# Performance work log

Measured on AMD Instinct MI355X. Metric: run time of the kernel, lower is better.

Reference implementation:

```python
import jax, jax.numpy as jnp
import numpy as np

DIM = 64
HEADS = 4            # self.num_heads = 2 * num_heads(=2)
SMK = 5
KS = 7
EPS = 1e-5
SCALE = (DIM // HEADS) ** -0.5


def pool_mat(n, out=7):
    # AdaptiveAvgPool2d bin matrix: P[i, j] = 1/size if floor(i*n/out) <= j < ceil((i+1)*n/out)
    P = np.zeros((out, n), np.float32)
    for i in range(out):
        s = (i * n) // out
        e = -((-(i + 1) * n) // out)
        P[i, s:e] = 1.0 / (e - s)
    return jnp.asarray(P)


def bn(x, g, b, m, v):
    # inference BatchNorm2d on [B,C,H,W]
    return (x - m[:, None, None]) * (g[:, None, None] * jax.lax.rsqrt(v[:, None, None] + EPS)) + b[:, None, None]


def conv1x1(x, w):
    return jnp.einsum('oi,bihw->bohw', w, x)


def rpb_bias(rpb, H, W, k):
    # replicate apply_rpb gather indexing (incl. the flip over flattened HW)
    rs = 2 * k - 1
    ih0 = np.arange(k)
    idx_k = (ih0[:, None] * rs + ih0[None, :]).reshape(-1)        # [k*k]
    rh = np.ones(k, np.int64); rh[k // 2] = H - (k - 1)
    rw = np.ones(k, np.int64); rw[k // 2] = W - (k - 1)
    ih = np.repeat(ih0, rh)                                       # [H]
    iw = np.repeat(ih0, rw)                                       # [W]
    bias_hw = ih[:, None] * rs + iw[None, :]                      # [H,W]
    bias_idx = (bias_hw[..., None] + idx_k).reshape(-1, k * k)[::-1].copy()  # [H*W,k*k]
    flat = rpb.reshape(rpb.shape[0], -1)                          # [G, rs*rs]
    return flat[:, bias_idx].reshape(1, rpb.shape[0], H, W, k * k)


def na2d_av(attn, value, k):
    # NATTEN-style neighborhood AV: window start clamped to stay in-bounds
    B, G, H, W, _ = attn.shape
    si = np.clip(np.arange(H) - k // 2, 0, H - k)
    sj = np.clip(np.arange(W) - k // 2, 0, W - k)
    ii = si[:, None] + np.arange(k)    # [H,k]
    jj = sj[:, None] + np.arange(k)    # [W,k]
    v = value[:, :, ii][:, :, :, :, jj]         # [B,G,H,k,W,k,C]
    a = attn.reshape(B, G, H, W, k, k)
    return jnp.einsum('bghwij,bghiwjc->bghwc', a, v)


def reference(x, wq_w, wq_g, wq_b, wq_m, wq_v,
              wk_w, wk_g, wk_b, wk_m, wk_v,
              proj_w, proj_b, rpb1, rpb2,
              dy_w, dy_g, dy_b, dy_m, dy_v):
    B, C, H, W = x.shape
    G = HEADS
    q, kctx = jnp.split(x, 2, axis=1)                      # [B,C/2,H,W] each
    q = bn(conv1x1(q, wq_w), wq_g, wq_b, wq_m, wq_v) * SCALE
    Ph, Pw = pool_mat(H), pool_mat(W)
    kp = jnp.einsum('ph,bchw,qw->bcpq', Ph, kctx, Pw)      # adaptive avg pool to 7x7
    k = bn(conv1x1(kp, wk_w), wk_g, wk_b, wk_m, wk_v)
    q = q.reshape(B, G, -1, H * W)                          # b g c n
    k = k.reshape(B, G, -1, 49)                             # b g c l
    w = jnp.einsum('bgcn,bgcl->bgnl', q, k)
    w = w.transpose(0, 3, 1, 2)                             # b l g n
    w = jnp.einsum('ol,blgn->bogn', proj_w, w) + proj_b[None, :, None, None]  # b (74) g n
    w = w.transpose(0, 2, 3, 1).reshape(B, G, H, W, SMK * SMK + KS * KS)
    attn1 = w[..., :SMK * SMK]
    attn2 = w[..., SMK * SMK:]
    attn1 = jax.nn.softmax(attn1 + rpb_bias(rpb1, H, W, SMK), axis=-1)
    attn2 = jax.nn.softmax(attn2 + rpb_bias(rpb2, H, W, KS), axis=-1)
    c = C // (2 * G)
    value = x.reshape(B, 2, G, c, H, W).transpose(1, 0, 2, 4, 5, 3)  # m b g h w c
    x1 = na2d_av(attn1, value[0], SMK)
    x2 = na2d_av(attn2, value[1], KS)
    out = jnp.concatenate([x1, x2], axis=1)                 # b (2g) h w c
    out = out.transpose(0, 1, 4, 2, 3).reshape(B, C, H, W)  # b (g c) h w
    return bn(conv1x1(out, dy_w), dy_g, dy_b, dy_m, dy_v)


def setup_inputs() -> dict:
    key = jax.random.key(0)
    ks = jax.random.split(key, 20)
    h = DIM // 2
    def bnp(k):
        k1, k2, k3, k4 = jax.random.split(k, 4)
        return (jax.random.uniform(k1, (0,)),)  # unused
    inp = {
        'x': jax.random.normal(ks[0], (8, DIM, 64, 64), jnp.float32),
        'wq_w': jax.random.normal(ks[1], (h, h), jnp.float32) * (h ** -0.5),
        'wq_g': jax.random.uniform(ks[2], (h,), jnp.float32, 0.5, 1.5),
        'wq_b': jax.random.normal(ks[3], (h,), jnp.float32) * 0.1,
        'wq_m': jax.random.normal(ks[4], (h,), jnp.float32) * 0.1,
        'wq_v': jax.random.uniform(ks[5], (h,), jnp.float32, 0.5, 1.5),
        'wk_w': jax.random.normal(ks[6], (h, h), jnp.float32) * (h ** -0.5),
        'wk_g': jax.random.uniform(ks[7], (h,), jnp.float32, 0.5, 1.5),
        'wk_b': jax.random.normal(ks[8], (h,), jnp.float32) * 0.1,
        'wk_m': jax.random.normal(ks[9], (h,), jnp.float32) * 0.1,
        'wk_v': jax.random.uniform(ks[10], (h,), jnp.float32, 0.5, 1.5),
        'proj_w': jax.random.normal(ks[11], (SMK * SMK + KS * KS, 49), jnp.float32) * (49 ** -0.5),
        'proj_b': jax.random.normal(ks[12], (SMK * SMK + KS * KS,), jnp.float32) * 0.02,
        'rpb1': jax.random.normal(ks[13], (HEADS, 2 * SMK - 1, 2 * SMK - 1), jnp.float32) * 0.02,
        'rpb2': jax.random.normal(ks[14], (HEADS, 2 * KS - 1, 2 * KS - 1), jnp.float32) * 0.02,
        'dy_w': jax.random.normal(ks[15], (DIM, DIM), jnp.float32) * (DIM ** -0.5),
        'dy_g': jax.random.uniform(ks[16], (DIM,), jnp.float32, 0.5, 1.5),
        'dy_b': jax.random.normal(ks[17], (DIM,), jnp.float32) * 0.1,
        'dy_m': jax.random.normal(ks[18], (DIM,), jnp.float32) * 0.1,
        'dy_v': jax.random.uniform(ks[19], (DIM,), jnp.float32, 0.5, 1.5),
    }
    return inp
```

## Files before the change

kernel.cpp:

```cpp
#include <hip/hip_runtime.h>

#define EPSV 1e-5f

#define OFF_W    12544
#define OFF_WQ2  31488
#define OFF_Q0   32512
#define OFF_DYT  32544

typedef float f4u __attribute__((ext_vector_type(4), aligned(4)));

__global__ __launch_bounds__(256) void pool_prep_kernel(
    const float* __restrict__ x,
    const float* __restrict__ wk_w, const float* __restrict__ wk_g,
    const float* __restrict__ wk_b, const float* __restrict__ wk_m,
    const float* __restrict__ wk_v,
    const float* __restrict__ wq_w, const float* __restrict__ wq_g,
    const float* __restrict__ wq_b, const float* __restrict__ wq_m,
    const float* __restrict__ wq_v,
    const float* __restrict__ dy_w,
    float* __restrict__ ws)
{
  __shared__ float s_tmp[32 * 64];
  __shared__ float s_kp[32 * 7];
  const int tid = threadIdx.x;

  if (blockIdx.x >= 56) {
    const int t = (blockIdx.x - 56) * 256 + tid;
    for (int idx = t; idx < 1056; idx += 2048) {
      if (idx < 1024) {
        const int i = idx >> 5, o = idx & 31;
        const float s = wq_g[o] * rsqrtf(wq_v[o] + EPSV);
        ws[OFF_WQ2 + idx] = 0.25f * s * wq_w[o * 32 + i];
      } else {
        const int o = idx - 1024;
        const float s = wq_g[o] * rsqrtf(wq_v[o] + EPSV);
        ws[OFF_Q0 + o] = 0.25f * (wq_b[o] - wq_m[o] * s);
      }
    }
    for (int idx = t; idx < 4096; idx += 2048) {
      const int i = idx >> 6, o = idx & 63;
      ws[OFF_DYT + idx] = dy_w[o * 64 + i];
    }
    return;
  }

  const int b = blockIdx.x / 7;
  const int p = blockIdx.x % 7;
  const int sh = (p * 64) / 7, eh = ((p + 1) * 64 + 6) / 7;
  const float invH = 1.0f / (float)(eh - sh);
  for (int idx = tid; idx < 2048; idx += 256) {
    const int c = idx >> 6, ww = idx & 63;
    const float* xp = x + ((size_t)(b * 64 + 32 + c)) * 4096 + ww;
    float s = 0.f;
    for (int hh = sh; hh < eh; ++hh) s += xp[hh * 64];
    s_tmp[idx] = s * invH;
  }
  __syncthreads();
  if (tid < 224) {
    const int c = tid / 7, q = tid % 7;
    const int sw = (q * 64) / 7, ew = ((q + 1) * 64 + 6) / 7;
    float s = 0.f;
    for (int ww = sw; ww < ew; ++ww) s += s_tmp[c * 64 + ww];
    s_kp[c * 7 + q] = s / (float)(ew - sw);
  }
  __syncthreads();
  if (tid < 224) {
    const int o = tid / 7, q = tid % 7;
    float s = 0.f;
#pragma unroll
    for (int i = 0; i < 32; i++) s += wk_w[o * 32 + i] * s_kp[i * 7 + q];
    const float sc = wk_g[o] * rsqrtf(wk_v[o] + EPSV);
    const int g = o >> 3, c = o & 7, l = p * 7 + q;
    ws[(((size_t)b * 4 + g) * 8 + c) * 49 + l] = (s - wk_m[o]) * sc + wk_b[o];
  }
}

__global__ __launch_bounds__(256) void fold_w_kernel(
    const float* __restrict__ proj_w, const float* __restrict__ ws_in,
    float* __restrict__ Wout)
{
  const int bg = blockIdx.x;
  const int tid = threadIdx.x;
  __shared__ float s_k[392];
  for (int i = tid; i < 392; i += 256) s_k[i] = ws_in[(size_t)bg * 392 + i];
  __syncthreads();
  for (int idx = tid; idx < 592; idx += 256) {
    const int o = idx >> 3, c = idx & 7;
    float s = 0.f;
#pragma unroll
    for (int l = 0; l < 49; l++) s += proj_w[o * 49 + l] * s_k[c * 49 + l];
    Wout[(size_t)bg * 592 + idx] = s;
  }
}

__global__ __launch_bounds__(512, 3) void contmix_main(
    const float* __restrict__ x,
    const float* __restrict__ proj_b,
    const float* __restrict__ rpb1, const float* __restrict__ rpb2,
    const float* __restrict__ dy_g, const float* __restrict__ dy_b,
    const float* __restrict__ dy_m, const float* __restrict__ dy_v,
    const float* __restrict__ ws,
    float* __restrict__ out)
{
  __shared__ float s_rpb1[4 * 81];
  __shared__ float s_rpb2[4 * 169];
  __shared__ float s_val[64 * 64];

  const int bx = blockIdx.x;
  const int b = bx >> 6;
  const int h = bx & 63;
  const int tid = threadIdx.x;
  const int w = tid & 63;
  const int bru = __builtin_amdgcn_readfirstlane(tid >> 8);
  const int gu  = __builtin_amdgcn_readfirstlane((tid >> 6) & 3);

  for (int i = tid; i < 324; i += 512) s_rpb1[i] = rpb1[i];
  for (int i = tid; i < 676; i += 512) s_rpb2[i] = rpb2[i];
  __syncthreads();

  const float* xb = x + (size_t)b * 64 * 4096;

  float q8[8];
  {
    const float* q0 = ws + OFF_Q0 + gu * 8;
#pragma unroll
    for (int o = 0; o < 8; o++) q8[o] = q0[o];
    const float* wq2 = ws + OFF_WQ2 + gu * 8;
#pragma unroll
    for (int i = 0; i < 32; i++) {
      const float xv = xb[i * 4096 + h * 64 + w];
#pragma unroll
      for (int o = 0; o < 8; o++) q8[o] += wq2[i * 32 + o] * xv;
    }
  }

  const float* Wr = ws + OFF_W + (size_t)(b * 4 + gu) * 592;
  const int ph = 63 - h, pw = 63 - w;

  if (bru == 0) {
    const int bih5 = ph - min(max(ph - 2, 0), 59);
    const int biw5 = pw - min(max(pw - 2, 0), 59);
    const int si5 = min(max(h - 2, 0), 59), sj5 = min(max(w - 2, 0), 59);
    float l1[25];
#pragma unroll
    for (int o = 0; o < 25; o++) {
      const float* wo = Wr + o * 8;
      float s = proj_b[o];
#pragma unroll
      for (int c = 0; c < 8; c++) s += wo[c] * q8[c];
      l1[o] = s;
    }
    const float* rp1 = s_rpb1 + gu * 81 + bih5 * 9 + biw5;
#pragma unroll
    for (int ki = 0; ki < 5; ki++)
#pragma unroll
      for (int kj = 0; kj < 5; kj++) l1[ki * 5 + kj] += rp1[ki * 9 + kj];

    float p0 = 0.f, p1 = 0.f, p2 = 0.f, p3 = 0.f;
#pragma unroll
    for (int o = 0; o < 25; o++) {
      const float e = __expf(l1[o]);
      l1[o] = e;
      if ((o & 3) == 0) p0 += e;
      else if ((o & 3) == 1) p1 += e;
      else if ((o & 3) == 2) p2 += e;
      else p3 += e;
    }
    const float inv = 1.f / ((p0 + p1) + (p2 + p3));

    float acc[8];
#pragma unroll
    for (int c = 0; c < 8; c++) acc[c] = 0.f;
    const float* vb = xb + gu * 8 * 4096;
#pragma unroll
    for (int i = 0; i < 5; i++) {
      const float a0 = l1[i * 5 + 0], a1 = l1[i * 5 + 1], a2 = l1[i * 5 + 2];
      const float a3 = l1[i * 5 + 3], a4 = l1[i * 5 + 4];
      const float* vr0 = vb + (si5 + i) * 64 + sj5;
#pragma unroll
      for (int c = 0; c < 8; c++) {
        const float* vr = vr0 + c * 4096;
        const f4u f = *(const f4u*)vr;
        const float v4 = vr[4];
        acc[c] += a0 * f.x + a1 * f.y + a2 * f.z + a3 * f.w + a4 * v4;
      }
    }
#pragma unroll
    for (int c = 0; c < 8; c++) s_val[(gu * 8 + c) * 64 + w] = acc[c] * inv;
  } else {
    const int bih7 = ph - min(max(ph - 3, 0), 57);
    const int biw7 = pw - min(max(pw - 3, 0), 57);
    const int si7 = min(max(h - 3, 0), 57), sj7 = min(max(w - 3, 0), 57);
    float l2[49];
#pragma unroll
    for (int o = 0; o < 49; o++) {
      const float* wo = Wr + (25 + o) * 8;
      float s = proj_b[25 + o];
#pragma unroll
      for (int c = 0; c < 8; c++) s += wo[c] * q8[c];
      l2[o] = s;
    }
    const float* rp2 = s_rpb2 + gu * 169 + bih7 * 13 + biw7;
#pragma unroll
    for (int ki = 0; ki < 7; ki++)
#pragma unroll
      for (int kj = 0; kj < 7; kj++) l2[ki * 7 + kj] += rp2[ki * 13 + kj];

    float p0 = 0.f, p1 = 0.f, p2 = 0.f, p3 = 0.f;
#pragma unroll
    for (int o = 0; o < 49; o++) {
      const float e = __expf(l2[o]);
      l2[o] = e;
      if ((o & 3) == 0) p0 += e;
      else if ((o & 3) == 1) p1 += e;
      else if ((o & 3) == 2) p2 += e;
      else p3 += e;
    }
    const float inv = 1.f / ((p0 + p1) + (p2 + p3));

    float acc[8];
#pragma unroll
    for (int c = 0; c < 8; c++) acc[c] = 0.f;
    const float* vb = xb + (32 + gu * 8) * 4096;
#pragma unroll
    for (int i = 0; i < 7; i++) {
      const float a0 = l2[i * 7 + 0], a1 = l2[i * 7 + 1], a2 = l2[i * 7 + 2];
      const float a3 = l2[i * 7 + 3], a4 = l2[i * 7 + 4], a5 = l2[i * 7 + 5];
      const float a6 = l2[i * 7 + 6];
      const float* vr0 = vb + (si7 + i) * 64 + sj7;
#pragma unroll
      for (int c = 0; c < 8; c++) {
        const float* vr = vr0 + c * 4096;
        const f4u fa = *(const f4u*)vr;
        const f4u fb = *(const f4u*)(vr + 3);
        acc[c] += a0 * fa.x + a1 * fa.y + a2 * fa.z + a3 * fa.w +
                  a4 * fb.y + a5 * fb.z + a6 * fb.w;
      }
    }
#pragma unroll
    for (int c = 0; c < 8; c++) s_val[(32 + gu * 8 + c) * 64 + w] = acc[c] * inv;
  }

  __syncthreads();

  {
    const int ogu = __builtin_amdgcn_readfirstlane(tid >> 6);
    float facc[8];
#pragma unroll
    for (int oo = 0; oo < 8; oo++) facc[oo] = 0.f;
    const float* dyt = ws + OFF_DYT + ogu * 8;
#pragma unroll
    for (int i = 0; i < 64; i++) {
      const float v = s_val[i * 64 + w];
#pragma unroll
      for (int oo = 0; oo < 8; oo++) facc[oo] += dyt[i * 64 + oo] * v;
    }
#pragma unroll
    for (int oo = 0; oo < 8; oo++) {
      const int oc = ogu * 8 + oo;
      const float sc = dy_g[oc] * rsqrtf(dy_v[oc] + EPSV);
      out[((size_t)(b * 64 + oc)) * 4096 + h * 64 + w] =
          (facc[oo] - dy_m[oc]) * sc + dy_b[oc];
    }
  }
}

extern "C" void kernel_launch(void* const* d_in, const int* in_sizes, int n_in,
                              void* d_out, int out_size, void* d_ws, size_t ws_size,
                              hipStream_t stream)
{
  const float* x      = (const float*)d_in[0];
  const float* wq_w   = (const float*)d_in[1];
  const float* wq_g   = (const float*)d_in[2];
  const float* wq_b   = (const float*)d_in[3];
  const float* wq_m   = (const float*)d_in[4];
  const float* wq_v   = (const float*)d_in[5];
  const float* wk_w   = (const float*)d_in[6];
  const float* wk_g   = (const float*)d_in[7];
  const float* wk_b   = (const float*)d_in[8];
  const float* wk_m   = (const float*)d_in[9];
  const float* wk_v   = (const float*)d_in[10];
  const float* proj_w = (const float*)d_in[11];
  const float* proj_b = (const float*)d_in[12];
  const float* rpb1   = (const float*)d_in[13];
  const float* rpb2   = (const float*)d_in[14];
  const float* dy_w   = (const float*)d_in[15];
  const float* dy_g   = (const float*)d_in[16];
  const float* dy_b   = (const float*)d_in[17];
  const float* dy_m   = (const float*)d_in[18];
  const float* dy_v   = (const float*)d_in[19];

  float* ws = (float*)d_ws;

  pool_prep_kernel<<<64, 256, 0, stream>>>(x, wk_w, wk_g, wk_b, wk_m, wk_v,
                                           wq_w, wq_g, wq_b, wq_m, wq_v,
                                           dy_w, ws);
  fold_w_kernel<<<32, 256, 0, stream>>>(proj_w, ws, ws + OFF_W);
  contmix_main<<<512, 512, 0, stream>>>(x, proj_b, rpb1, rpb2,
                                        dy_g, dy_b, dy_m, dy_v,
                                        ws, (float*)d_out);
}
```

Measured before the change: 173.1 us.

## Split attention window rows across two thread halves with shared-memory softmax merge

Doubles the block size to 1024 threads and splits each neighborhood window's rows between two half-blocks. Each half computes partial exp-sums and AV accumulations, which are merged through shared memory before normalization. The final 1x1 projection is spread over twice as many waves with 4 outputs each. The aim is more parallelism and less register pressure per thread. The cost is recomputing q8 in both halves, an extra barrier and extra shared-memory traffic.

```diff
diff --git a/kernel.cpp b/kernel.cpp
--- a/kernel.cpp
+++ b/kernel.cpp
@@ -93,7 +93,64 @@
   }
 }
 
-__global__ __launch_bounds__(512, 3) void contmix_main(
+template <int K, int R0, int R1, int PBASE>
+__device__ __forceinline__ void attn_part(
+    const float* __restrict__ Wr, const float* __restrict__ proj_b,
+    const float* __restrict__ rp, const float* __restrict__ vb,
+    int si, int sj, const float* q8, float* acc, float& den)
+{
+  constexpr int RS = 2 * K - 1;
+  constexpr int NP = (R1 - R0) * K;
+  float l[NP];
+#pragma unroll
+  for (int i = R0; i < R1; i++)
+#pragma unroll
+    for (int j = 0; j < K; j++) {
+      const int p = i * K + j;
+      const float* wo = Wr + (PBASE + p) * 8;
+      float s = proj_b[PBASE + p];
+#pragma unroll
+      for (int c = 0; c < 8; c++) s += wo[c] * q8[c];
+      l[(i - R0) * K + j] = s + rp[i * RS + j];
+    }
+  float p0 = 0.f, p1 = 0.f, p2 = 0.f, p3 = 0.f;
+#pragma unroll
+  for (int o = 0; o < NP; o++) {
+    const float e = __expf(l[o]);
+    l[o] = e;
+    if ((o & 3) == 0) p0 += e;
+    else if ((o & 3) == 1) p1 += e;
+    else if ((o & 3) == 2) p2 += e;
+    else p3 += e;
+  }
+  den = (p0 + p1) + (p2 + p3);
+#pragma unroll
+  for (int c = 0; c < 8; c++) acc[c] = 0.f;
+#pragma unroll
+  for (int i = R0; i < R1; i++) {
+    const float* vr0 = vb + (si + i) * 64 + sj;
+#pragma unroll
+    for (int c = 0; c < 8; c++) {
+      const float* vr = vr0 + c * 4096;
+      if constexpr (K == 5) {
+        const f4u f = *(const f4u*)vr;
+        const float v4 = vr[4];
+        acc[c] += l[(i - R0) * 5 + 0] * f.x + l[(i - R0) * 5 + 1] * f.y +
+                  l[(i - R0) * 5 + 2] * f.z + l[(i - R0) * 5 + 3] * f.w +
+                  l[(i - R0) * 5 + 4] * v4;
+      } else {
+        const f4u fa = *(const f4u*)vr;
+        const f4u fb = *(const f4u*)(vr + 3);
+        acc[c] += l[(i - R0) * 7 + 0] * fa.x + l[(i - R0) * 7 + 1] * fa.y +
+                  l[(i - R0) * 7 + 2] * fa.z + l[(i - R0) * 7 + 3] * fa.w +
+                  l[(i - R0) * 7 + 4] * fb.y + l[(i - R0) * 7 + 5] * fb.z +
+                  l[(i - R0) * 7 + 6] * fb.w;
+      }
+    }
+  }
+}
+
+__global__ __launch_bounds__(1024, 4) void contmix_main(
     const float* __restrict__ x,
     const float* __restrict__ proj_b,
     const float* __restrict__ rpb1, const float* __restrict__ rpb2,
@@ -102,20 +159,21 @@
     const float* __restrict__ ws,
     float* __restrict__ out)
 {
-  __shared__ float s_rpb1[4 * 81];
-  __shared__ float s_rpb2[4 * 169];
   __shared__ float s_val[64 * 64];
-
-  const int bx = blockIdx.x;
-  const int b = bx >> 6;
-  const int h = bx & 63;
+  __shared__ float s_den[512];
+  __shared__ float s_rpb1[324];
+  __shared__ float s_rpb2[676];
+
+  const int b = blockIdx.x >> 6;
+  const int h = blockIdx.x & 63;
   const int tid = threadIdx.x;
   const int w = tid & 63;
-  const int bru = __builtin_amdgcn_readfirstlane(tid >> 8);
   const int gu  = __builtin_amdgcn_readfirstlane((tid >> 6) & 3);
-
-  for (int i = tid; i < 324; i += 512) s_rpb1[i] = rpb1[i];
-  for (int i = tid; i < 676; i += 512) s_rpb2[i] = rpb2[i];
+  const int bru = __builtin_amdgcn_readfirstlane((tid >> 8) & 1);
+  const int hfu = __builtin_amdgcn_readfirstlane(tid >> 9);
+
+  for (int i = tid; i < 324; i += 1024) s_rpb1[i] = rpb1[i];
+  for (int i = tid; i < 676; i += 1024) s_rpb2[i] = rpb2[i];
   __syncthreads();
 
   const float* xb = x + (size_t)b * 64 * 4096;
@@ -137,127 +195,61 @@
   const float* Wr = ws + OFF_W + (size_t)(b * 4 + gu) * 592;
   const int ph = 63 - h, pw = 63 - w;
 
+  float acc[8];
+  float den;
   if (bru == 0) {
-    const int bih5 = ph - min(max(ph - 2, 0), 59);
-    const int biw5 = pw - min(max(pw - 2, 0), 59);
-    const int si5 = min(max(h - 2, 0), 59), sj5 = min(max(w - 2, 0), 59);
-    float l1[25];
-#pragma unroll
-    for (int o = 0; o < 25; o++) {
-      const float* wo = Wr + o * 8;
-      float s = proj_b[o];
-#pragma unroll
-      for (int c = 0; c < 8; c++) s += wo[c] * q8[c];
-      l1[o] = s;
-    }
-    const float* rp1 = s_rpb1 + gu * 81 + bih5 * 9 + biw5;
-#pragma unroll
-    for (int ki = 0; ki < 5; ki++)
-#pragma unroll
-      for (int kj = 0; kj < 5; kj++) l1[ki * 5 + kj] += rp1[ki * 9 + kj];
-
-    float p0 = 0.f, p1 = 0.f, p2 = 0.f, p3 = 0.f;
-#pragma unroll
-    for (int o = 0; o < 25; o++) {
-      const float e = __expf(l1[o]);
-      l1[o] = e;
-      if ((o & 3) == 0) p0 += e;
-      else if ((o & 3) == 1) p1 += e;
-      else if ((o & 3) == 2) p2 += e;
-      else p3 += e;
-    }
-    const float inv = 1.f / ((p0 + p1) + (p2 + p3));
-
-    float acc[8];
-#pragma unroll
-    for (int c = 0; c < 8; c++) acc[c] = 0.f;
+    const int bih = ph - min(max(ph - 2, 0), 59);
+    const int biw = pw - min(max(pw - 2, 0), 59);
+    const int si = min(max(h - 2, 0), 59), sj = min(max(w - 2, 0), 59);
+    const float* rp = s_rpb1 + gu * 81 + bih * 9 + biw;
     const float* vb = xb + gu * 8 * 4096;
-#pragma unroll
-    for (int i = 0; i < 5; i++) {
-      const float a0 = l1[i * 5 + 0], a1 = l1[i * 5 + 1], a2 = l1[i * 5 + 2];
-      const float a3 = l1[i * 5 + 3], a4 = l1[i * 5 + 4];
-      const float* vr0 = vb + (si5 + i) * 64 + sj5;
-#pragma unroll
-      for (int c = 0; c < 8; c++) {
-        const float* vr = vr0 + c * 4096;
-        const f4u f = *(const f4u*)vr;
-        const float v4 = vr[4];
-        acc[c] += a0 * f.x + a1 * f.y + a2 * f.z + a3 * f.w + a4 * v4;
-      }
-    }
-#pragma unroll
-    for (int c = 0; c < 8; c++) s_val[(gu * 8 + c) * 64 + w] = acc[c] * inv;
+    if (hfu == 0)
+      attn_part<5, 0, 3, 0>(Wr, proj_b, rp, vb, si, sj, q8, acc, den);
+    else
+      attn_part<5, 3, 5, 0>(Wr, proj_b, rp, vb, si, sj, q8, acc, den);
   } else {
-    const int bih7 = ph - min(max(ph - 3, 0), 57);
-    const int biw7 = pw - min(max(pw - 3, 0), 57);
-    const int si7 = min(max(h - 3, 0), 57), sj7 = min(max(w - 3, 0), 57);
-    float l2[49];
-#pragma unroll
-    for (int o = 0; o < 49; o++) {
-      const float* wo = Wr + (25 + o) * 8;
-      float s = proj_b[25 + o];
-#pragma unroll
-      for (int c = 0; c < 8; c++) s += wo[c] * q8[c];
-      l2[o] = s;
-    }
-    const float* rp2 = s_rpb2 + gu * 169 + bih7 * 13 + biw7;
-#pragma unroll
-    for (int ki = 0; ki < 7; ki++)
-#pragma unroll
-      for (int kj = 0; kj < 7; kj++) l2[ki * 7 + kj] += rp2[ki * 13 + kj];
-
-    float p0 = 0.f, p1 = 0.f, p2 = 0.f, p3 = 0.f;
-#pragma unroll
-    for (int o = 0; o < 49; o++) {
-      const float e = __expf(l2[o]);
-      l2[o] = e;
-      if ((o & 3) == 0) p0 += e;
-      else if ((o & 3) == 1) p1 += e;
-      else if ((o & 3) == 2) p2 += e;
-      else p3 += e;
-    }
-    const float inv = 1.f / ((p0 + p1) + (p2 + p3));
-
-    float acc[8];
-#pragma unroll
-    for (int c = 0; c < 8; c++) acc[c] = 0.f;
+    const int bih = ph - min(max(ph - 3, 0), 57);
+    const int biw = pw - min(max(pw - 3, 0), 57);
+    const int si = min(max(h - 3, 0), 57), sj = min(max(w - 3, 0), 57);
+    const float* rp = s_rpb2 + gu * 169 + bih * 13 + biw;
     const float* vb = xb + (32 + gu * 8) * 4096;
-#pragma unroll
-    for (int i = 0; i < 7; i++) {
-      const float a0 = l2[i * 7 + 0], a1 = l2[i * 7 + 1], a2 = l2[i * 7 + 2];
-      const float a3 = l2[i * 7 + 3], a4 = l2[i * 7 + 4], a5 = l2[i * 7 + 5];
-      const float a6 = l2[i * 7 + 6];
-      const float* vr0 = vb + (si7 + i) * 64 + sj7;
-#pragma unroll
-      for (int c = 0; c < 8; c++) {
-        const float* vr = vr0 + c * 4096;
-        const f4u fa = *(const f4u*)vr;
-        const f4u fb = *(const f4u*)(vr + 3);
-        acc[c] += a0 * fa.x + a1 * fa.y + a2 * fa.z + a3 * fa.w +
-                  a4 * fb.y + a5 * fb.z + a6 * fb.w;
-      }
-    }
-#pragma unroll
-    for (int c = 0; c < 8; c++) s_val[(32 + gu * 8 + c) * 64 + w] = acc[c] * inv;
-  }
-
+    if (hfu == 0)
+      attn_part<7, 0, 4, 25>(Wr, proj_b, rp, vb, si, sj, q8, acc, den);
+    else
+      attn_part<7, 4, 7, 25>(Wr, proj_b, rp, vb, si, sj, q8, acc, den);
+  }
+
+  const int chbase = bru * 32 + gu * 8;
+  if (hfu == 0) {
+    s_den[(bru * 4 + gu) * 64 + w] = den;
+#pragma unroll
+    for (int c = 0; c < 8; c++) s_val[(chbase + c) * 64 + w] = acc[c];
+  }
+  __syncthreads();
+  if (hfu == 1) {
+    const float inv = 1.f / (s_den[(bru * 4 + gu) * 64 + w] + den);
+#pragma unroll
+    for (int c = 0; c < 8; c++)
+      s_val[(chbase + c) * 64 + w] =
+          (s_val[(chbase + c) * 64 + w] + acc[c]) * inv;
+  }
   __syncthreads();
 
   {
-    const int ogu = __builtin_amdgcn_readfirstlane(tid >> 6);
-    float facc[8];
-#pragma unroll
-    for (int oo = 0; oo < 8; oo++) facc[oo] = 0.f;
-    const float* dyt = ws + OFF_DYT + ogu * 8;
+    const int og = __builtin_amdgcn_readfirstlane(tid >> 6);
+    float facc[4];
+#pragma unroll
+    for (int oo = 0; oo < 4; oo++) facc[oo] = 0.f;
+    const float* dyt = ws + OFF_DYT + og * 4;
 #pragma unroll
     for (int i = 0; i < 64; i++) {
       const float v = s_val[i * 64 + w];
 #pragma unroll
-      for (int oo = 0; oo < 8; oo++) facc[oo] += dyt[i * 64 + oo] * v;
-    }
-#pragma unroll
-    for (int oo = 0; oo < 8; oo++) {
-      const int oc = ogu * 8 + oo;
+      for (int oo = 0; oo < 4; oo++) facc[oo] += dyt[i * 64 + oo] * v;
+    }
+#pragma unroll
+    for (int oo = 0; oo < 4; oo++) {
+      const int oc = og * 4 + oo;
       const float sc = dy_g[oc] * rsqrtf(dy_v[oc] + EPSV);
       out[((size_t)(b * 64 + oc)) * 4096 + h * 64 + w] =
           (facc[oo] - dy_m[oc]) * sc + dy_b[oc];
@@ -296,7 +288,7 @@
                                            wq_w, wq_g, wq_b, wq_m, wq_v,
                                            dy_w, ws);
   fold_w_kernel<<<32, 256, 0, stream>>>(proj_w, ws, ws + OFF_W);
-  contmix_main<<<512, 512, 0, stream>>>(x, proj_b, rpb1, rpb2,
-                                        dy_g, dy_b, dy_m, dy_v,
-                                        ws, (float*)d_out);
-}
+  contmix_main<<<512, 1024, 0, stream>>>(x, proj_b, rpb1, rpb2,
+                                         dy_g, dy_b, dy_m, dy_v,
+                                         ws, (float*)d_out);
+}
```

Measured after the change: 173.3 us. No clear change (+0.1%).
